# Kernel tuning notes

Hardware: AMD Instinct MI355X
Metric: run time of the kernel (lower is better)

## Reference

```python
import jax, jax.numpy as jnp
import numpy as np

N_FEATURES = 16384
N_EXPERTS = 8
D_IN = 768
EXPERT_DIM = N_FEATURES // N_EXPERTS  # 2048
N_TOKENS = 16384


def setup_inputs() -> dict:
    key = jax.random.key(0)
    k_act, k_preb, k_enc, k_dec, k_rb, k_r = jax.random.split(key, 6)
    activations = jax.random.normal(k_act, (N_TOKENS, D_IN), dtype=jnp.float32)
    pre_b = jax.random.normal(k_preb, (D_IN,), dtype=jnp.float32) * 0.01
    enc = jax.random.normal(k_enc, (N_EXPERTS, D_IN, EXPERT_DIM), dtype=jnp.float32) / (2.0 ** 0.5) / (D_IN ** 0.5)
    dec = jax.random.normal(k_dec, (N_EXPERTS, EXPERT_DIM, D_IN), dtype=jnp.float32) / (EXPERT_DIM ** 0.5)
    router_b = jax.random.normal(k_rb, (D_IN,), dtype=jnp.float32) * 0.01
    router = jax.random.normal(k_r, (D_IN, N_EXPERTS), dtype=jnp.float32) / (D_IN ** 0.5)
    return {"activations": activations, "pre_b": pre_b, "enc": enc, "dec": dec,
            "router_b": router_b, "router": router}


def reference(activations, pre_b, enc, dec, router_b, router):
    # Router: softmax over experts, top-1 routing.
    logits = (activations - router_b) @ router            # [N, E]
    probs = jax.nn.softmax(logits, axis=-1)
    expert_max_prob = jnp.max(probs, axis=-1)              # [N]
    expert_idx = jnp.argmax(probs, axis=-1)                # [N] int

    n_experts = enc.shape[0]
    recons = jnp.zeros_like(activations)
    # Fixed small loop over experts; tokens are masked (zeroed) per expert so
    # each per-expert encode/decode GEMM only contributes for its routed rows.
    for e in range(n_experts):
        mask = (expert_idx == e)[:, None]                  # [N, 1]
        x_e = jnp.where(mask, activations, 0.0)            # masked gather
        latent = jax.nn.relu(x_e @ enc[e])                 # [N, expert_dim]
        recon = latent @ dec[e]                            # [N, d_in]
        recons = recons + jnp.where(mask, recon, 0.0)      # scatter-combine

    return expert_max_prob[:, None] * recons + pre_b
```

## Files before the change

kernel.cpp:

```cpp
#include <hip/hip_runtime.h>
#include <hip/hip_bf16.h>
#include <hip/hip_fp16.h>

#define N_TOKENS 16384
#define D_IN 768
#define N_EXPERTS 8
#define EXPERT_DIM 2048

#define ROUTER_BLOCKS 256
#define TOK_PER_BLOCK 64

typedef _Float16 half8 __attribute__((ext_vector_type(8)));
typedef _Float16 half4 __attribute__((ext_vector_type(4)));
typedef float floatx4 __attribute__((ext_vector_type(4)));


#define WAIT_VM8  0xF78
#define WAIT_VM4  0xF74
#define WAIT_VM0  0xF70

__device__ __forceinline__ void glds16(const _Float16* g, _Float16* l) {
    __builtin_amdgcn_global_load_lds(
        (const __attribute__((address_space(1))) unsigned int*)g,
        (__attribute__((address_space(3))) unsigned int*)l, 16, 0, 0);
}

__global__ __launch_bounds__(256) void router_convert(const float* __restrict__ act,
    const float* __restrict__ router_b, const float* __restrict__ router,
    _Float16* __restrict__ act_h, float* __restrict__ prob, int* __restrict__ localpos,
    int* __restrict__ eidx, int* __restrict__ hist)
{
    __shared__ int h[N_EXPERTS];
    if (threadIdx.x < N_EXPERTS) h[threadIdx.x] = 0;
    __syncthreads();

    int wave = threadIdx.x >> 6, lane = threadIdx.x & 63;

    float rb[3][4];
#pragma unroll
    for (int c = 0; c < 3; ++c) {
        float4 v = *(const float4*)(router_b + lane * 4 + c * 256);
        rb[c][0] = v.x; rb[c][1] = v.y; rb[c][2] = v.z; rb[c][3] = v.w;
    }

#pragma unroll 1
    for (int it = 0; it < 16; ++it) {
        int t = blockIdx.x * TOK_PER_BLOCK + wave * 16 + it;
        const float* arow = act + (size_t)t * D_IN;
        float acc[8];
#pragma unroll
        for (int e = 0; e < 8; ++e) acc[e] = 0.f;
#pragma unroll
        for (int c = 0; c < 3; ++c) {
            int i0 = lane * 4 + c * 256;
            float4 v = *(const float4*)(arow + i0);
            half4 hv;
            hv[0] = (_Float16)v.x; hv[1] = (_Float16)v.y;
            hv[2] = (_Float16)v.z; hv[3] = (_Float16)v.w;
            *(half4*)(act_h + (size_t)t * D_IN + i0) = hv;
            float va[4] = {v.x, v.y, v.z, v.w};
#pragma unroll
            for (int q = 0; q < 4; ++q) {
                float a = va[q] - rb[c][q];
                const float* r = router + (size_t)(i0 + q) * 8;
#pragma unroll
                for (int e = 0; e < 8; ++e) acc[e] += a * r[e];
            }
        }
#pragma unroll
        for (int s = 32; s > 0; s >>= 1) {
#pragma unroll
            for (int e = 0; e < 8; ++e) acc[e] += __shfl_down(acc[e], s, 64);
        }
        if (lane == 0) {
            float m = acc[0]; int ai = 0;
#pragma unroll
            for (int e = 1; e < 8; ++e) if (acc[e] > m) { m = acc[e]; ai = e; }
            float s = 0.f;
#pragma unroll
            for (int e = 0; e < 8; ++e) s += __expf(acc[e] - m);
            prob[t] = 1.0f / s;
            eidx[t] = ai;
            localpos[t] = atomicAdd(&h[ai], 1);
        }
    }
    __syncthreads();
    if (threadIdx.x < N_EXPERTS) hist[blockIdx.x * N_EXPERTS + threadIdx.x] = h[threadIdx.x];
}

__global__ __launch_bounds__(256) void scan_kernel(int* __restrict__ hist,
    int* __restrict__ counts, int* __restrict__ offsets)
{
    __shared__ int sh[ROUTER_BLOCKS * N_EXPERTS];
    __shared__ int tot[N_EXPERTS], off[N_EXPERTS];
    int tid = threadIdx.x;
    *(int4*)&sh[tid * 8]     = *(const int4*)&hist[tid * 8];
    *(int4*)&sh[tid * 8 + 4] = *(const int4*)&hist[tid * 8 + 4];
    __syncthreads();
    if (tid < N_EXPERTS) {
        int run = 0;
        for (int b = 0; b < ROUTER_BLOCKS; ++b) {
            int v = sh[b * 8 + tid];
            sh[b * 8 + tid] = run;
            run += v;
        }
        tot[tid] = run;
    }
    __syncthreads();
    if (tid == 0) {
        int run = 0;
        for (int e = 0; e < N_EXPERTS; ++e) {
            off[e] = run; offsets[e] = run; counts[e] = tot[e]; run += tot[e];
        }
    }
    __syncthreads();
    int4 a = *(const int4*)&sh[tid * 8];
    int4 b = *(const int4*)&sh[tid * 8 + 4];
    a.x += off[0]; a.y += off[1]; a.z += off[2]; a.w += off[3];
    b.x += off[4]; b.y += off[5]; b.z += off[6]; b.w += off[7];
    *(int4*)&hist[tid * 8]     = a;
    *(int4*)&hist[tid * 8 + 4] = b;
}

__global__ __launch_bounds__(256) void order_kernel(const int* __restrict__ eidx,
    const int* __restrict__ localpos, const int* __restrict__ hist,
    int* __restrict__ order)
{
    int t = blockIdx.x * 256 + threadIdx.x;
    int base = hist[(t >> 6) * N_EXPERTS + eidx[t]];
    order[base + localpos[t]] = t;
}

__global__ __launch_bounds__(256) void transpose_both(const float* __restrict__ enc,
    const float* __restrict__ dec, _Float16* __restrict__ encT, _Float16* __restrict__ decT)
{
    __shared__ _Float16 tile[64][72];
    int id = blockIdx.x;
    const float* W; _Float16* WT; int K, Nc, bx, by, bz;
    if (id < 3072) {
        W = enc; WT = encT; K = D_IN; Nc = EXPERT_DIM;
        bx = id & 31; by = (id >> 5) % 12; bz = id / 384;
    } else {
        int id2 = id - 3072;
        W = dec; WT = decT; K = EXPERT_DIM; Nc = D_IN;
        bx = id2 % 12; by = (id2 / 12) & 31; bz = id2 / 384;
    }
    size_t esz = (size_t)K * Nc;
    const float* We = W + (size_t)bz * esz;
    _Float16* WTe = WT + (size_t)bz * esz;
    int n0 = bx * 64, k0 = by * 64;
    int tr = threadIdx.x >> 4;
    int tc = threadIdx.x & 15;
#pragma unroll
    for (int rr = 0; rr < 64; rr += 16) {
        int k = k0 + rr + tr;
        float4 v = *(const float4*)(We + (size_t)k * Nc + n0 + tc * 4);
        tile[tc * 4 + 0][rr + tr] = (_Float16)v.x;
        tile[tc * 4 + 1][rr + tr] = (_Float16)v.y;
        tile[tc * 4 + 2][rr + tr] = (_Float16)v.z;
        tile[tc * 4 + 3][rr + tr] = (_Float16)v.w;
    }
    __syncthreads();
#pragma unroll
    for (int p = 0; p < 2; ++p) {
        int idp = threadIdx.x + p * 256;
        int r = idp >> 3, ch = idp & 7;
        half8 v = *(const half8*)&tile[r][ch * 8];
        *(half8*)(WTe + (size_t)(n0 + r) * K + k0 + ch * 8) = v;
    }
}

#define STAGE_A(bufp, k0h)                                      \
    do {                                                        \
        glds16(pa0 + (k0h), (bufp) + st_base);                  \
        glds16(pa1 + (k0h), (bufp) + st_base + 512);            \
    } while (0)
#define STAGE_B(bufp, k0h)                                      \
    do {                                                        \
        glds16(pb0 + (k0h), (bufp) + 8192 + st_base);           \
        glds16(pb1 + (k0h), (bufp) + 8192 + st_base + 512);     \
    } while (0)

__global__ __launch_bounds__(512, 2) void encode_kernel(const _Float16* __restrict__ act_h,
    const _Float16* __restrict__ encT, const int* __restrict__ order,
    const int* __restrict__ counts, const int* __restrict__ offsets,
    _Float16* __restrict__ latent)
{
    int id = blockIdx.x;
    int e = id & 7;
    int j = id >> 3;
    int nt = j & 7;
    int mt = j >> 3;

    int n_e = counts[e];
    if (mt * 256 >= n_e) return;
    int slot0 = offsets[e] + mt * 256;
    int mrem = n_e - mt * 256;

    __shared__ _Float16 lds[4][16384];
    __shared__ int s_tok[256];

    int tid = threadIdx.x;
    if (tid < 256) s_tok[tid] = (tid < mrem) ? order[slot0 + tid] : order[slot0];
    __syncthreads();

    int w = tid >> 6, lane = tid & 63;
    int wm = w >> 2, wn = w & 3;
    int mrow = lane & 15;

    int st_base = w * 1024 + lane * 8;
    int c_st = ((lane & 3) - ((lane >> 3) & 3)) & 3;
    int r_in = lane >> 2;
    const _Float16* Be = encT + (size_t)e * D_IN * EXPERT_DIM + (size_t)(nt * 256) * D_IN;
    const _Float16* pa0 = act_h + (size_t)s_tok[w * 32 + r_in] * D_IN + c_st * 8;
    const _Float16* pa1 = act_h + (size_t)s_tok[w * 32 + 16 + r_in] * D_IN + c_st * 8;
    const _Float16* pb0 = Be + (size_t)(w * 32 + r_in) * D_IN + c_st * 8;
    const _Float16* pb1 = Be + (size_t)(w * 32 + 16 + r_in) * D_IN + c_st * 8;

    int fo = (((lane >> 4) + (mrow >> 1)) & 3) * 8;
    int aoff = (wm * 128 + mrow) * 32 + fo;
    int boff = 8192 + (wn * 64 + mrow) * 32 + fo;

    floatx4 acc[8][4];
#pragma unroll
    for (int i = 0; i < 8; ++i)
#pragma unroll
        for (int jj = 0; jj < 4; ++jj) acc[i][jj] = (floatx4){0.f, 0.f, 0.f, 0.f};

    const int T = D_IN / 32;
    STAGE_A(&lds[0][0], 0);  STAGE_B(&lds[0][0], 0);
    STAGE_A(&lds[1][0], 32); STAGE_B(&lds[1][0], 32);
    STAGE_A(&lds[2][0], 64); STAGE_B(&lds[2][0], 64);
    __builtin_amdgcn_s_waitcnt(WAIT_VM8);
    __builtin_amdgcn_s_barrier();

#pragma unroll 1
    for (int t = 0; t < T; ++t) {
        _Float16* cur = &lds[t & 3][0];
        _Float16* nx3 = &lds[(t + 3) & 3][0];
        int k3 = (t + 3) * 32;
        half8 af0[4], bf[4];
#pragma unroll
        for (int i = 0; i < 4; ++i) af0[i] = *(const half8*)&cur[aoff + i * 512];
#pragma unroll
        for (int jj = 0; jj < 4; ++jj) bf[jj] = *(const half8*)&cur[boff + jj * 512];
        if (t + 3 < T) STAGE_A(nx3, k3);
        __builtin_amdgcn_s_barrier();
        __builtin_amdgcn_s_setprio(1);
#pragma unroll
        for (int i = 0; i < 4; ++i)
#pragma unroll
            for (int jj = 0; jj < 4; ++jj)
                acc[i][jj] = __builtin_amdgcn_mfma_f32_16x16x32_f16(af0[i], bf[jj], acc[i][jj], 0, 0, 0);
        __builtin_amdgcn_s_setprio(0);
        __builtin_amdgcn_s_barrier();
        half8 af1[4];
#pragma unroll
        for (int i = 0; i < 4; ++i) af1[i] = *(const half8*)&cur[aoff + (i + 4) * 512];
        if (t + 3 < T) STAGE_B(nx3, k3);
        __builtin_amdgcn_s_barrier();
        __builtin_amdgcn_s_setprio(1);
#pragma unroll
        for (int i = 0; i < 4; ++i)
#pragma unroll
            for (int jj = 0; jj < 4; ++jj)
                acc[i + 4][jj] = __builtin_amdgcn_mfma_f32_16x16x32_f16(af1[i], bf[jj], acc[i + 4][jj], 0, 0, 0);
        __builtin_amdgcn_s_setprio(0);
        if (t + 1 < T) {
            if (t + 3 < T)      __builtin_amdgcn_s_waitcnt(WAIT_VM8);
            else if (t + 2 < T) __builtin_amdgcn_s_waitcnt(WAIT_VM4);
            else                __builtin_amdgcn_s_waitcnt(WAIT_VM0);
            __builtin_amdgcn_s_barrier();
        }
    }

#pragma unroll
    for (int i = 0; i < 8; ++i) {
        int row0 = wm * 128 + i * 16 + (lane >> 4) * 4;
#pragma unroll
        for (int jj = 0; jj < 4; ++jj) {
            int col = nt * 256 + wn * 64 + jj * 16 + mrow;
#pragma unroll
            for (int r = 0; r < 4; ++r) {
                int row = row0 + r;
                if (row < mrem) {
                    float v = acc[i][jj][r];
                    v = v > 0.f ? v : 0.f;
                    latent[(size_t)(slot0 + row) * EXPERT_DIM + col] = (_Float16)v;
                }
            }
        }
    }
}

__global__ __launch_bounds__(512, 2) void decode_kernel(const _Float16* __restrict__ latent,
    const _Float16* __restrict__ decT, const int* __restrict__ order,
    const int* __restrict__ counts, const int* __restrict__ offsets,
    const float* __restrict__ prob, const float* __restrict__ pre_b,
    float* __restrict__ out)
{
    int id = blockIdx.x;
    int e = id & 7;
    int j = id >> 3;
    int nt = j % 3;
    int mt = j / 3;

    int n_e = counts[e];
    if (mt * 256 >= n_e) return;
    int slot0 = offsets[e] + mt * 256;
    int mrem = n_e - mt * 256;

    __shared__ _Float16 lds[4][16384];
    __shared__ int s_tok[256];
    __shared__ float s_p[256];

    int tid = threadIdx.x;
    if (tid < 256) {
        int tok = (tid < mrem) ? order[slot0 + tid] : order[slot0];
        s_tok[tid] = tok;
        s_p[tid] = prob[tok];
    }
    __syncthreads();

    int w = tid >> 6, lane = tid & 63;
    int wm = w >> 2, wn = w & 3;
    int mrow = lane & 15;

    int st_base = w * 1024 + lane * 8;
    int c_st = ((lane & 3) - ((lane >> 3) & 3)) & 3;
    int r_in = lane >> 2;
    const _Float16* Ae = latent + (size_t)slot0 * EXPERT_DIM;
    const _Float16* Be = decT + (size_t)e * EXPERT_DIM * D_IN + (size_t)(nt * 256) * EXPERT_DIM;
    const _Float16* pa0 = Ae + (size_t)(w * 32 + r_in) * EXPERT_DIM + c_st * 8;
    const _Float16* pa1 = Ae + (size_t)(w * 32 + 16 + r_in) * EXPERT_DIM + c_st * 8;
    const _Float16* pb0 = Be + (size_t)(w * 32 + r_in) * EXPERT_DIM + c_st * 8;
    const _Float16* pb1 = Be + (size_t)(w * 32 + 16 + r_in) * EXPERT_DIM + c_st * 8;

    int fo = (((lane >> 4) + (mrow >> 1)) & 3) * 8;
    int aoff = (wm * 128 + mrow) * 32 + fo;
    int boff = 8192 + (wn * 64 + mrow) * 32 + fo;

    floatx4 acc[8][4];
#pragma unroll
    for (int i = 0; i < 8; ++i)
#pragma unroll
        for (int jj = 0; jj < 4; ++jj) acc[i][jj] = (floatx4){0.f, 0.f, 0.f, 0.f};

    const int T = EXPERT_DIM / 32;
    STAGE_A(&lds[0][0], 0);  STAGE_B(&lds[0][0], 0);
    STAGE_A(&lds[1][0], 32); STAGE_B(&lds[1][0], 32);
    STAGE_A(&lds[2][0], 64); STAGE_B(&lds[2][0], 64);
    __builtin_amdgcn_s_waitcnt(WAIT_VM8);
    __builtin_amdgcn_s_barrier();

#pragma unroll 1
    for (int t = 0; t < T; ++t) {
        _Float16* cur = &lds[t & 3][0];
        _Float16* nx3 = &lds[(t + 3) & 3][0];
        int k3 = (t + 3) * 32;
        half8 af0[4], bf[4];
#pragma unroll
        for (int i = 0; i < 4; ++i) af0[i] = *(const half8*)&cur[aoff + i * 512];
#pragma unroll
        for (int jj = 0; jj < 4; ++jj) bf[jj] = *(const half8*)&cur[boff + jj * 512];
        if (t + 3 < T) STAGE_A(nx3, k3);
        __builtin_amdgcn_s_barrier();
        __builtin_amdgcn_s_setprio(1);
#pragma unroll
        for (int i = 0; i < 4; ++i)
#pragma unroll
            for (int jj = 0; jj < 4; ++jj)
                acc[i][jj] = __builtin_amdgcn_mfma_f32_16x16x32_f16(af0[i], bf[jj], acc[i][jj], 0, 0, 0);
        __builtin_amdgcn_s_setprio(0);
        __builtin_amdgcn_s_barrier();
        half8 af1[4];
#pragma unroll
        for (int i = 0; i < 4; ++i) af1[i] = *(const half8*)&cur[aoff + (i + 4) * 512];
        if (t + 3 < T) STAGE_B(nx3, k3);
        __builtin_amdgcn_s_barrier();
        __builtin_amdgcn_s_setprio(1);
#pragma unroll
        for (int i = 0; i < 4; ++i)
#pragma unroll
            for (int jj = 0; jj < 4; ++jj)
                acc[i + 4][jj] = __builtin_amdgcn_mfma_f32_16x16x32_f16(af1[i], bf[jj], acc[i + 4][jj], 0, 0, 0);
        __builtin_amdgcn_s_setprio(0);
        if (t + 1 < T) {
            if (t + 3 < T)      __builtin_amdgcn_s_waitcnt(WAIT_VM8);
            else if (t + 2 < T) __builtin_amdgcn_s_waitcnt(WAIT_VM4);
            else                __builtin_amdgcn_s_waitcnt(WAIT_VM0);
            __builtin_amdgcn_s_barrier();
        }
    }

#pragma unroll
    for (int i = 0; i < 8; ++i) {
        int row0 = wm * 128 + i * 16 + (lane >> 4) * 4;
#pragma unroll
        for (int jj = 0; jj < 4; ++jj) {
            int col = nt * 256 + wn * 64 + jj * 16 + mrow;
            float pb = pre_b[col];
#pragma unroll
            for (int r = 0; r < 4; ++r) {
                int row = row0 + r;
                if (row < mrem) {
                    out[(size_t)s_tok[row] * D_IN + col] = s_p[row] * acc[i][jj][r] + pb;
                }
            }
        }
    }
}

extern "C" void kernel_launch(void* const* d_in, const int* in_sizes, int n_in,
                              void* d_out, int out_size, void* d_ws, size_t ws_size,
                              hipStream_t stream)
{
    const float* act      = (const float*)d_in[0];
    const float* pre_b    = (const float*)d_in[1];
    const float* enc      = (const float*)d_in[2];
    const float* dec      = (const float*)d_in[3];
    const float* router_b = (const float*)d_in[4];
    const float* router   = (const float*)d_in[5];
    float* out = (float*)d_out;

    char* w = (char*)d_ws;
    int* counts  = (int*)w;  w += 256;
    int* offsets = (int*)w;  w += 256;
    int* hist    = (int*)w;  w += ROUTER_BLOCKS * N_EXPERTS * 4;
    int* eidx    = (int*)w;  w += N_TOKENS * 4;
    int* lpos    = (int*)w;  w += N_TOKENS * 4;
    int* order   = (int*)w;  w += N_TOKENS * 4;
    float* prob  = (float*)w; w += N_TOKENS * 4;
    _Float16* act_h  = (_Float16*)w; w += (size_t)N_TOKENS * D_IN * 2;
    _Float16* encT   = (_Float16*)w; w += (size_t)N_EXPERTS * D_IN * EXPERT_DIM * 2;
    _Float16* decT   = (_Float16*)w; w += (size_t)N_EXPERTS * D_IN * EXPERT_DIM * 2;
    _Float16* latent = (_Float16*)w; w += (size_t)(N_TOKENS + 256) * EXPERT_DIM * 2;

    router_convert<<<ROUTER_BLOCKS, 256, 0, stream>>>(act, router_b, router, act_h, prob, lpos, eidx, hist);
    scan_kernel<<<1, 256, 0, stream>>>(hist, counts, offsets);
    order_kernel<<<N_TOKENS / 256, 256, 0, stream>>>(eidx, lpos, hist, order);

    transpose_both<<<6144, 256, 0, stream>>>(enc, dec, encT, decT);

    encode_kernel<<<4096, 512, 0, stream>>>(act_h, encT, order, counts, offsets, latent);
    decode_kernel<<<1536, 512, 0, stream>>>(latent, decT, order, counts, offsets, prob, pre_b, out);
}
```

Baseline: 370.7 us.

## Fuse router with weight transpose, merge scan into order, vectorize GEMM epilogues

```diff
diff --git a/kernel.cpp b/kernel.cpp
--- a/kernel.cpp
+++ b/kernel.cpp
@@ -25,125 +25,84 @@
         (__attribute__((address_space(3))) unsigned int*)l, 16, 0, 0);
 }
 
-__global__ __launch_bounds__(256) void router_convert(const float* __restrict__ act,
+__global__ __launch_bounds__(256) void prep_kernel(const float* __restrict__ act,
     const float* __restrict__ router_b, const float* __restrict__ router,
+    const float* __restrict__ enc, const float* __restrict__ dec,
     _Float16* __restrict__ act_h, float* __restrict__ prob, int* __restrict__ localpos,
-    int* __restrict__ eidx, int* __restrict__ hist)
-{
-    __shared__ int h[N_EXPERTS];
-    if (threadIdx.x < N_EXPERTS) h[threadIdx.x] = 0;
-    __syncthreads();
-
-    int wave = threadIdx.x >> 6, lane = threadIdx.x & 63;
-
-    float rb[3][4];
-#pragma unroll
-    for (int c = 0; c < 3; ++c) {
-        float4 v = *(const float4*)(router_b + lane * 4 + c * 256);
-        rb[c][0] = v.x; rb[c][1] = v.y; rb[c][2] = v.z; rb[c][3] = v.w;
-    }
-
-#pragma unroll 1
-    for (int it = 0; it < 16; ++it) {
-        int t = blockIdx.x * TOK_PER_BLOCK + wave * 16 + it;
-        const float* arow = act + (size_t)t * D_IN;
-        float acc[8];
-#pragma unroll
-        for (int e = 0; e < 8; ++e) acc[e] = 0.f;
-#pragma unroll
-        for (int c = 0; c < 3; ++c) {
-            int i0 = lane * 4 + c * 256;
-            float4 v = *(const float4*)(arow + i0);
-            half4 hv;
-            hv[0] = (_Float16)v.x; hv[1] = (_Float16)v.y;
-            hv[2] = (_Float16)v.z; hv[3] = (_Float16)v.w;
-            *(half4*)(act_h + (size_t)t * D_IN + i0) = hv;
-            float va[4] = {v.x, v.y, v.z, v.w};
-#pragma unroll
-            for (int q = 0; q < 4; ++q) {
-                float a = va[q] - rb[c][q];
-                const float* r = router + (size_t)(i0 + q) * 8;
-#pragma unroll
-                for (int e = 0; e < 8; ++e) acc[e] += a * r[e];
-            }
-        }
-#pragma unroll
-        for (int s = 32; s > 0; s >>= 1) {
-#pragma unroll
-            for (int e = 0; e < 8; ++e) acc[e] += __shfl_down(acc[e], s, 64);
-        }
-        if (lane == 0) {
-            float m = acc[0]; int ai = 0;
-#pragma unroll
-            for (int e = 1; e < 8; ++e) if (acc[e] > m) { m = acc[e]; ai = e; }
-            float s = 0.f;
-#pragma unroll
-            for (int e = 0; e < 8; ++e) s += __expf(acc[e] - m);
-            prob[t] = 1.0f / s;
-            eidx[t] = ai;
-            localpos[t] = atomicAdd(&h[ai], 1);
-        }
-    }
-    __syncthreads();
-    if (threadIdx.x < N_EXPERTS) hist[blockIdx.x * N_EXPERTS + threadIdx.x] = h[threadIdx.x];
-}
-
-__global__ __launch_bounds__(256) void scan_kernel(int* __restrict__ hist,
-    int* __restrict__ counts, int* __restrict__ offsets)
-{
-    __shared__ int sh[ROUTER_BLOCKS * N_EXPERTS];
-    __shared__ int tot[N_EXPERTS], off[N_EXPERTS];
-    int tid = threadIdx.x;
-    *(int4*)&sh[tid * 8]     = *(const int4*)&hist[tid * 8];
-    *(int4*)&sh[tid * 8 + 4] = *(const int4*)&hist[tid * 8 + 4];
-    __syncthreads();
-    if (tid < N_EXPERTS) {
-        int run = 0;
-        for (int b = 0; b < ROUTER_BLOCKS; ++b) {
-            int v = sh[b * 8 + tid];
-            sh[b * 8 + tid] = run;
-            run += v;
-        }
-        tot[tid] = run;
-    }
-    __syncthreads();
-    if (tid == 0) {
-        int run = 0;
-        for (int e = 0; e < N_EXPERTS; ++e) {
-            off[e] = run; offsets[e] = run; counts[e] = tot[e]; run += tot[e];
-        }
-    }
-    __syncthreads();
-    int4 a = *(const int4*)&sh[tid * 8];
-    int4 b = *(const int4*)&sh[tid * 8 + 4];
-    a.x += off[0]; a.y += off[1]; a.z += off[2]; a.w += off[3];
-    b.x += off[4]; b.y += off[5]; b.z += off[6]; b.w += off[7];
-    *(int4*)&hist[tid * 8]     = a;
-    *(int4*)&hist[tid * 8 + 4] = b;
-}
-
-__global__ __launch_bounds__(256) void order_kernel(const int* __restrict__ eidx,
-    const int* __restrict__ localpos, const int* __restrict__ hist,
-    int* __restrict__ order)
-{
-    int t = blockIdx.x * 256 + threadIdx.x;
-    int base = hist[(t >> 6) * N_EXPERTS + eidx[t]];
-    order[base + localpos[t]] = t;
-}
-
-__global__ __launch_bounds__(256) void transpose_both(const float* __restrict__ enc,
-    const float* __restrict__ dec, _Float16* __restrict__ encT, _Float16* __restrict__ decT)
+    int* __restrict__ eidx, int* __restrict__ hist,
+    _Float16* __restrict__ encT, _Float16* __restrict__ decT)
 {
     __shared__ _Float16 tile[64][72];
+    __shared__ int h[N_EXPERTS];
     int id = blockIdx.x;
+
+    if (id < ROUTER_BLOCKS) {
+        if (threadIdx.x < N_EXPERTS) h[threadIdx.x] = 0;
+        __syncthreads();
+
+        int wave = threadIdx.x >> 6, lane = threadIdx.x & 63;
+        float rb[3][4];
+#pragma unroll
+        for (int c = 0; c < 3; ++c) {
+            float4 v = *(const float4*)(router_b + lane * 4 + c * 256);
+            rb[c][0] = v.x; rb[c][1] = v.y; rb[c][2] = v.z; rb[c][3] = v.w;
+        }
+
+#pragma unroll 1
+        for (int it = 0; it < 16; ++it) {
+            int t = id * TOK_PER_BLOCK + wave * 16 + it;
+            const float* arow = act + (size_t)t * D_IN;
+            float acc[8];
+#pragma unroll
+            for (int e = 0; e < 8; ++e) acc[e] = 0.f;
+#pragma unroll
+            for (int c = 0; c < 3; ++c) {
+                int i0 = lane * 4 + c * 256;
+                float4 v = *(const float4*)(arow + i0);
+                half4 hv;
+                hv[0] = (_Float16)v.x; hv[1] = (_Float16)v.y;
+                hv[2] = (_Float16)v.z; hv[3] = (_Float16)v.w;
+                *(half4*)(act_h + (size_t)t * D_IN + i0) = hv;
+                float va[4] = {v.x, v.y, v.z, v.w};
+#pragma unroll
+                for (int q = 0; q < 4; ++q) {
+                    float a = va[q] - rb[c][q];
+                    const float* r = router + (size_t)(i0 + q) * 8;
+#pragma unroll
+                    for (int e = 0; e < 8; ++e) acc[e] += a * r[e];
+                }
+            }
+#pragma unroll
+            for (int s = 32; s > 0; s >>= 1) {
+#pragma unroll
+                for (int e = 0; e < 8; ++e) acc[e] += __shfl_down(acc[e], s, 64);
+            }
+            if (lane == 0) {
+                float m = acc[0]; int ai = 0;
+#pragma unroll
+                for (int e = 1; e < 8; ++e) if (acc[e] > m) { m = acc[e]; ai = e; }
+                float s = 0.f;
+#pragma unroll
+                for (int e = 0; e < 8; ++e) s += __expf(acc[e] - m);
+                prob[t] = 1.0f / s;
+                eidx[t] = ai;
+                localpos[t] = atomicAdd(&h[ai], 1);
+            }
+        }
+        __syncthreads();
+        if (threadIdx.x < N_EXPERTS) hist[id * N_EXPERTS + threadIdx.x] = h[threadIdx.x];
+        return;
+    }
+
+    int id2 = id - ROUTER_BLOCKS;
     const float* W; _Float16* WT; int K, Nc, bx, by, bz;
-    if (id < 3072) {
+    if (id2 < 3072) {
         W = enc; WT = encT; K = D_IN; Nc = EXPERT_DIM;
-        bx = id & 31; by = (id >> 5) % 12; bz = id / 384;
+        bx = id2 & 31; by = (id2 >> 5) % 12; bz = id2 / 384;
     } else {
-        int id2 = id - 3072;
+        int id3 = id2 - 3072;
         W = dec; WT = decT; K = EXPERT_DIM; Nc = D_IN;
-        bx = id2 % 12; by = (id2 / 12) & 31; bz = id2 / 384;
+        bx = id3 % 12; by = (id3 / 12) & 31; bz = id3 / 384;
     }
     size_t esz = (size_t)K * Nc;
     const float* We = W + (size_t)bz * esz;
@@ -168,6 +127,51 @@
         half8 v = *(const half8*)&tile[r][ch * 8];
         *(half8*)(WTe + (size_t)(n0 + r) * K + k0 + ch * 8) = v;
     }
+}
+
+__global__ __launch_bounds__(256) void order_scan_kernel(const int* __restrict__ eidx,
+    const int* __restrict__ localpos, const int* __restrict__ hist,
+    int* __restrict__ order, int* __restrict__ counts, int* __restrict__ offsets)
+{
+    __shared__ int sh[ROUTER_BLOCKS * N_EXPERTS];
+    int tid = threadIdx.x;
+    int4 a = ((const int4*)hist)[tid * 2];
+    int4 b = ((const int4*)hist)[tid * 2 + 1];
+    int o[8] = {a.x, a.y, a.z, a.w, b.x, b.y, b.z, b.w};
+    int v[8];
+#pragma unroll
+    for (int e = 0; e < 8; ++e) { v[e] = o[e]; sh[tid * 8 + e] = v[e]; }
+    __syncthreads();
+#pragma unroll 1
+    for (int s = 1; s < 256; s <<= 1) {
+        int t2[8];
+        if (tid >= s) {
+#pragma unroll
+            for (int e = 0; e < 8; ++e) t2[e] = sh[(tid - s) * 8 + e];
+        }
+        __syncthreads();
+        if (tid >= s) {
+#pragma unroll
+            for (int e = 0; e < 8; ++e) { v[e] += t2[e]; sh[tid * 8 + e] = v[e]; }
+        }
+        __syncthreads();
+    }
+    int tot[8];
+#pragma unroll
+    for (int e = 0; e < 8; ++e) tot[e] = sh[255 * 8 + e];
+    int eo[8]; int run = 0;
+#pragma unroll
+    for (int e = 0; e < 8; ++e) { eo[e] = run; run += tot[e]; }
+    __syncthreads();
+#pragma unroll
+    for (int e = 0; e < 8; ++e) sh[tid * 8 + e] = eo[e] + v[e] - o[e];
+    __syncthreads();
+
+    if (blockIdx.x == 0 && tid < 8) { counts[tid] = tot[tid]; offsets[tid] = eo[tid]; }
+
+    int t = blockIdx.x * 256 + tid;
+    int base = sh[(t >> 6) * 8 + eidx[t]];
+    order[base + localpos[t]] = t;
 }
 
 #define STAGE_A(bufp, k0h)                                      \
@@ -205,7 +209,8 @@
     __syncthreads();
 
     int w = tid >> 6, lane = tid & 63;
-    int wm = w >> 2, wn = w & 3;
+    int wm_n = w >> 2;
+    int wn_m = w & 3;
     int mrow = lane & 15;
 
     int st_base = w * 1024 + lane * 8;
@@ -218,8 +223,8 @@
     const _Float16* pb1 = Be + (size_t)(w * 32 + 16 + r_in) * D_IN + c_st * 8;
 
     int fo = (((lane >> 4) + (mrow >> 1)) & 3) * 8;
-    int aoff = (wm * 128 + mrow) * 32 + fo;
-    int boff = 8192 + (wn * 64 + mrow) * 32 + fo;
+    int moff = (wn_m * 64 + mrow) * 32 + fo;
+    int noff = 8192 + (wm_n * 128 + mrow) * 32 + fo;
 
     floatx4 acc[8][4];
 #pragma unroll
@@ -239,11 +244,11 @@
         _Float16* cur = &lds[t & 3][0];
         _Float16* nx3 = &lds[(t + 3) & 3][0];
         int k3 = (t + 3) * 32;
-        half8 af0[4], bf[4];
-#pragma unroll
-        for (int i = 0; i < 4; ++i) af0[i] = *(const half8*)&cur[aoff + i * 512];
-#pragma unroll
-        for (int jj = 0; jj < 4; ++jj) bf[jj] = *(const half8*)&cur[boff + jj * 512];
+        half8 mf[4], nf0[4];
+#pragma unroll
+        for (int jj = 0; jj < 4; ++jj) mf[jj] = *(const half8*)&cur[moff + jj * 512];
+#pragma unroll
+        for (int i = 0; i < 4; ++i) nf0[i] = *(const half8*)&cur[noff + i * 512];
         if (t + 3 < T) STAGE_A(nx3, k3);
         __builtin_amdgcn_s_barrier();
         __builtin_amdgcn_s_setprio(1);
@@ -251,12 +256,12 @@
         for (int i = 0; i < 4; ++i)
 #pragma unroll
             for (int jj = 0; jj < 4; ++jj)
-                acc[i][jj] = __builtin_amdgcn_mfma_f32_16x16x32_f16(af0[i], bf[jj], acc[i][jj], 0, 0, 0);
+                acc[i][jj] = __builtin_amdgcn_mfma_f32_16x16x32_f16(nf0[i], mf[jj], acc[i][jj], 0, 0, 0);
         __builtin_amdgcn_s_setprio(0);
         __builtin_amdgcn_s_barrier();
-        half8 af1[4];
-#pragma unroll
-        for (int i = 0; i < 4; ++i) af1[i] = *(const half8*)&cur[aoff + (i + 4) * 512];
+        half8 nf1[4];
+#pragma unroll
+        for (int i = 0; i < 4; ++i) nf1[i] = *(const half8*)&cur[noff + (i + 4) * 512];
         if (t + 3 < T) STAGE_B(nx3, k3);
         __builtin_amdgcn_s_barrier();
         __builtin_amdgcn_s_setprio(1);
@@ -264,7 +269,7 @@
         for (int i = 0; i < 4; ++i)
 #pragma unroll
             for (int jj = 0; jj < 4; ++jj)
-                acc[i + 4][jj] = __builtin_amdgcn_mfma_f32_16x16x32_f16(af1[i], bf[jj], acc[i + 4][jj], 0, 0, 0);
+                acc[i + 4][jj] = __builtin_amdgcn_mfma_f32_16x16x32_f16(nf1[i], mf[jj], acc[i + 4][jj], 0, 0, 0);
         __builtin_amdgcn_s_setprio(0);
         if (t + 1 < T) {
             if (t + 3 < T)      __builtin_amdgcn_s_waitcnt(WAIT_VM8);
@@ -276,18 +281,18 @@
 
 #pragma unroll
     for (int i = 0; i < 8; ++i) {
-        int row0 = wm * 128 + i * 16 + (lane >> 4) * 4;
+        int ncol = nt * 256 + wm_n * 128 + i * 16 + (lane >> 4) * 4;
 #pragma unroll
         for (int jj = 0; jj < 4; ++jj) {
-            int col = nt * 256 + wn * 64 + jj * 16 + mrow;
-#pragma unroll
-            for (int r = 0; r < 4; ++r) {
-                int row = row0 + r;
-                if (row < mrem) {
+            int m_row = wn_m * 64 + jj * 16 + mrow;
+            if (m_row < mrem) {
+                half4 hv;
+#pragma unroll
+                for (int r = 0; r < 4; ++r) {
                     float v = acc[i][jj][r];
-                    v = v > 0.f ? v : 0.f;
-                    latent[(size_t)(slot0 + row) * EXPERT_DIM + col] = (_Float16)v;
+                    hv[r] = (_Float16)(v > 0.f ? v : 0.f);
                 }
+                *(half4*)(latent + (size_t)(slot0 + m_row) * EXPERT_DIM + ncol) = hv;
             }
         }
     }
@@ -323,7 +328,8 @@
     __syncthreads();
 
     int w = tid >> 6, lane = tid & 63;
-    int wm = w >> 2, wn = w & 3;
+    int wm_n = w >> 2;
+    int wn_m = w & 3;
     int mrow = lane & 15;
 
     int st_base = w * 1024 + lane * 8;
@@ -337,8 +343,8 @@
     const _Float16* pb1 = Be + (size_t)(w * 32 + 16 + r_in) * EXPERT_DIM + c_st * 8;
 
     int fo = (((lane >> 4) + (mrow >> 1)) & 3) * 8;
-    int aoff = (wm * 128 + mrow) * 32 + fo;
-    int boff = 8192 + (wn * 64 + mrow) * 32 + fo;
+    int moff = (wn_m * 64 + mrow) * 32 + fo;
+    int noff = 8192 + (wm_n * 128 + mrow) * 32 + fo;
 
     floatx4 acc[8][4];
 #pragma unroll
@@ -358,11 +364,11 @@
         _Float16* cur = &lds[t & 3][0];
         _Float16* nx3 = &lds[(t + 3) & 3][0];
         int k3 = (t + 3) * 32;
-        half8 af0[4], bf[4];
-#pragma unroll
-        for (int i = 0; i < 4; ++i) af0[i] = *(const half8*)&cur[aoff + i * 512];
-#pragma unroll
-        for (int jj = 0; jj < 4; ++jj) bf[jj] = *(const half8*)&cur[boff + jj * 512];
+        half8 mf[4], nf0[4];
+#pragma unroll
+        for (int jj = 0; jj < 4; ++jj) mf[jj] = *(const half8*)&cur[moff + jj * 512];
+#pragma unroll
+        for (int i = 0; i < 4; ++i) nf0[i] = *(const half8*)&cur[noff + i * 512];
         if (t + 3 < T) STAGE_A(nx3, k3);
         __builtin_amdgcn_s_barrier();
         __builtin_amdgcn_s_setprio(1);
@@ -370,12 +376,12 @@
         for (int i = 0; i < 4; ++i)
 #pragma unroll
             for (int jj = 0; jj < 4; ++jj)
-                acc[i][jj] = __builtin_amdgcn_mfma_f32_16x16x32_f16(af0[i], bf[jj], acc[i][jj], 0, 0, 0);
+                acc[i][jj] = __builtin_amdgcn_mfma_f32_16x16x32_f16(nf0[i], mf[jj], acc[i][jj], 0, 0, 0);
         __builtin_amdgcn_s_setprio(0);
         __builtin_amdgcn_s_barrier();
-        half8 af1[4];
-#pragma unroll
-        for (int i = 0; i < 4; ++i) af1[i] = *(const half8*)&cur[aoff + (i + 4) * 512];
+        half8 nf1[4];
+#pragma unroll
+        for (int i = 0; i < 4; ++i) nf1[i] = *(const half8*)&cur[noff + (i + 4) * 512];
         if (t + 3 < T) STAGE_B(nx3, k3);
         __builtin_amdgcn_s_barrier();
         __builtin_amdgcn_s_setprio(1);
@@ -383,7 +389,7 @@
         for (int i = 0; i < 4; ++i)
 #pragma unroll
             for (int jj = 0; jj < 4; ++jj)
-                acc[i + 4][jj] = __builtin_amdgcn_mfma_f32_16x16x32_f16(af1[i], bf[jj], acc[i + 4][jj], 0, 0, 0);
+                acc[i + 4][jj] = __builtin_amdgcn_mfma_f32_16x16x32_f16(nf1[i], mf[jj], acc[i + 4][jj], 0, 0, 0);
         __builtin_amdgcn_s_setprio(0);
         if (t + 1 < T) {
             if (t + 3 < T)      __builtin_amdgcn_s_waitcnt(WAIT_VM8);
@@ -395,17 +401,19 @@
 
 #pragma unroll
     for (int i = 0; i < 8; ++i) {
-        int row0 = wm * 128 + i * 16 + (lane >> 4) * 4;
+        int ncol = nt * 256 + wm_n * 128 + i * 16 + (lane >> 4) * 4;
+        float4 pb = *(const float4*)(pre_b + ncol);
 #pragma unroll
         for (int jj = 0; jj < 4; ++jj) {
-            int col = nt * 256 + wn * 64 + jj * 16 + mrow;
-            float pb = pre_b[col];
-#pragma unroll
-            for (int r = 0; r < 4; ++r) {
-                int row = row0 + r;
-                if (row < mrem) {
-                    out[(size_t)s_tok[row] * D_IN + col] = s_p[row] * acc[i][jj][r] + pb;
-                }
+            int m_row = wn_m * 64 + jj * 16 + mrow;
+            if (m_row < mrem) {
+                float sp = s_p[m_row];
+                float4 ov;
+                ov.x = sp * acc[i][jj][0] + pb.x;
+                ov.y = sp * acc[i][jj][1] + pb.y;
+                ov.z = sp * acc[i][jj][2] + pb.z;
+                ov.w = sp * acc[i][jj][3] + pb.w;
+                *(float4*)(out + (size_t)s_tok[m_row] * D_IN + ncol) = ov;
             }
         }
     }
@@ -436,12 +444,9 @@
     _Float16* decT   = (_Float16*)w; w += (size_t)N_EXPERTS * D_IN * EXPERT_DIM * 2;
     _Float16* latent = (_Float16*)w; w += (size_t)(N_TOKENS + 256) * EXPERT_DIM * 2;
 
-    router_convert<<<ROUTER_BLOCKS, 256, 0, stream>>>(act, router_b, router, act_h, prob, lpos, eidx, hist);
-    scan_kernel<<<1, 256, 0, stream>>>(hist, counts, offsets);
-    order_kernel<<<N_TOKENS / 256, 256, 0, stream>>>(eidx, lpos, hist, order);
-
-    transpose_both<<<6144, 256, 0, stream>>>(enc, dec, encT, decT);
-
+    prep_kernel<<<6400, 256, 0, stream>>>(act, router_b, router, enc, dec,
+                                          act_h, prob, lpos, eidx, hist, encT, decT);
+    order_scan_kernel<<<N_TOKENS / 256, 256, 0, stream>>>(eidx, lpos, hist, order, counts, offsets);
     encode_kernel<<<4096, 512, 0, stream>>>(act_h, encT, order, counts, offsets, latent);
     decode_kernel<<<1536, 512, 0, stream>>>(latent, decT, order, counts, offsets, prob, pre_b, out);
 }
```

New measurement: 367.3 us. No clear change (-0.9%).
